# Kernel tuning notes

Measured on AMD Instinct MI355X. Metric: run time of the kernel, lower is better.

## Reference

```python
import jax, jax.numpy as jnp
import numpy as np

B, S, D, H, Dh, F = 1, 2048, 2048, 24, 128, 8192  # batch, seq, dim, heads, dim_head, ff hidden
SCALE = Dh ** -0.5


def _layernorm(x, g, b, eps=1e-5):
    mu = jnp.mean(x, axis=-1, keepdims=True)
    var = jnp.var(x, axis=-1, keepdims=True)
    return (x - mu) * jax.lax.rsqrt(var + eps) * g + b


def _rmsnorm(x, g, eps=1e-5):
    ms = jnp.mean(jnp.square(x), axis=-1, keepdims=True)
    return x * jax.lax.rsqrt(ms + eps) * g


def setup_inputs() -> dict:
    key = jax.random.key(0)
    ks = jax.random.split(key, 8)
    w = lambda k, sh: (jax.random.normal(k, sh, jnp.float32) * (1.0 / np.sqrt(sh[0]))).astype(jnp.float32)
    return {
        "x": jax.random.normal(ks[0], (B, S, D), jnp.float32),
        "ln_g": jnp.ones((D,), jnp.float32),
        "ln_b": jnp.zeros((D,), jnp.float32),
        "attn_g": jnp.ones((D,), jnp.float32),  # RingAttention prenorm (RMSNorm) gamma
        "Wq": w(ks[1], (D, H * Dh)),
        "Wk": w(ks[2], (D, H * Dh)),
        "Wv": w(ks[3], (D, H * Dh)),
        "Wo": w(ks[4], (H * Dh, D)),
        "W1": w(ks[5], (D, F)),
        "b1": jnp.zeros((F,), jnp.float32),
        "W2": w(ks[6], (F, D)),
        "b2": jnp.zeros((D,), jnp.float32),
    }


def reference(x, ln_g, ln_b, attn_g, Wq, Wk, Wv, Wo, W1, b1, W2, b2):
    # outer block LayerNorm
    x = _layernorm(x, ln_g, ln_b)

    # --- causal multi-head attention (math-equivalent to ring attention) ---
    h = _rmsnorm(x, attn_g)  # attention's internal prenorm
    q = (h @ Wq).reshape(B, S, H, Dh)
    k = (h @ Wk).reshape(B, S, H, Dh)
    v = (h @ Wv).reshape(B, S, H, Dh)
    scores = jnp.einsum("bqhd,bkhd->bhqk", q, k) * SCALE  # [B,H,S,S]
    causal = jnp.tril(jnp.ones((S, S), bool))
    scores = jnp.where(causal, scores, jnp.finfo(scores.dtype).min)
    attn = jax.nn.softmax(scores, axis=-1)
    o = jnp.einsum("bhqk,bkhd->bqhd", attn, v).reshape(B, S, H * Dh)
    x = o @ Wo + x  # residual

    # --- feedforward + residual ---
    x = jax.nn.gelu(x @ W1 + b1) @ W2 + b2 + x
    return x
```

## Files before the change

kernel.cpp:

```cpp
#include <hip/hip_runtime.h>
#include <hip/hip_bf16.h>

#define Sq 2048
#define Dm 2048
#define HDim 3072
#define QKVDim 9216
#define NH 24
#define DH 128
#define FF 8192
#define ATT_SCALE 0.08838834764831845f

using bf16 = __hip_bfloat16;
typedef __attribute__((ext_vector_type(8))) short bf16x8;
typedef __attribute__((ext_vector_type(4))) float f32x4;
typedef unsigned int u32;
typedef unsigned long long u64;
typedef __attribute__((ext_vector_type(4))) u32 u32x4;

__device__ __forceinline__ void gload_lds16(const void* g, void* l) {
    __builtin_amdgcn_global_load_lds(
        (const __attribute__((address_space(1))) void*)g,
        (__attribute__((address_space(3))) void*)l, 16, 0, 0);
}

__global__ __launch_bounds__(256) void ln_rms_kernel(
    const float* __restrict__ x, const float* __restrict__ g, const float* __restrict__ b,
    const float* __restrict__ ag, float* __restrict__ xnf, bf16* __restrict__ h)
{
    __shared__ float redA[4], redB[4], redC[4];
    int row = blockIdx.x;
    int t = threadIdx.x;
    int lane = t & 63, wid = t >> 6;
    const float* xr = x + (size_t)row * Dm;

    float v[8];
    float sum = 0.f, ssq = 0.f;
#pragma unroll
    for (int i = 0; i < 8; i++) {
        float f = xr[t + 256 * i];
        v[i] = f; sum += f; ssq += f * f;
    }
#pragma unroll
    for (int off = 32; off > 0; off >>= 1) {
        sum += __shfl_down(sum, off);
        ssq += __shfl_down(ssq, off);
    }
    if (lane == 0) { redA[wid] = sum; redB[wid] = ssq; }
    __syncthreads();
    sum = redA[0] + redA[1] + redA[2] + redA[3];
    ssq = redB[0] + redB[1] + redB[2] + redB[3];
    float mu = sum * (1.f / Dm);
    float var = ssq * (1.f / Dm) - mu * mu;
    float rstd = rsqrtf(var + 1e-5f);

    float xn[8];
    float s2 = 0.f;
#pragma unroll
    for (int i = 0; i < 8; i++) {
        int col = t + 256 * i;
        float xv = (v[i] - mu) * rstd * g[col] + b[col];
        xn[i] = xv;
        xnf[(size_t)row * Dm + col] = xv;
        s2 += xv * xv;
    }
#pragma unroll
    for (int off = 32; off > 0; off >>= 1) s2 += __shfl_down(s2, off);
    if (lane == 0) redC[wid] = s2;
    __syncthreads();
    s2 = redC[0] + redC[1] + redC[2] + redC[3];
    float rms = rsqrtf(s2 * (1.f / Dm) + 1e-5f);
#pragma unroll
    for (int i = 0; i < 8; i++) {
        int col = t + 256 * i;
        h[(size_t)row * Dm + col] = __float2bfloat16(xn[i] * rms * ag[col]);
    }
}

__global__ __launch_bounds__(256) void transpose_cvt_kernel(
    const float* __restrict__ W, bf16* __restrict__ Wt, int K, int N)
{
    __shared__ float tile[32][36];
    int n0 = blockIdx.x * 32, k0 = blockIdx.y * 32;
    int t = threadIdx.x;
    int r = t >> 3, c4 = (t & 7) * 4;
    f32x4 v = *reinterpret_cast<const f32x4*>(W + (size_t)(k0 + r) * N + n0 + c4);
    *reinterpret_cast<f32x4*>(&tile[r][c4]) = v;
    __syncthreads();
    int nr = t >> 3, kc = (t & 7) * 4;
    bf16 o4[4];
    o4[0] = __float2bfloat16(tile[kc + 0][nr]);
    o4[1] = __float2bfloat16(tile[kc + 1][nr]);
    o4[2] = __float2bfloat16(tile[kc + 2][nr]);
    o4[3] = __float2bfloat16(tile[kc + 3][nr]);
    *reinterpret_cast<u64*>(Wt + (size_t)(n0 + nr) * K + k0 + kc) = *reinterpret_cast<const u64*>(o4);
}

__global__ __launch_bounds__(256) void transpose_cvt3_kernel(
    const float* __restrict__ Wa, const float* __restrict__ Wb, const float* __restrict__ Wc,
    bf16* __restrict__ Wt, int K, int N)
{
    __shared__ float tile[32][36];
    const float* W = blockIdx.z == 0 ? Wa : (blockIdx.z == 1 ? Wb : Wc);
    bf16* dst = Wt + (size_t)blockIdx.z * N * K;
    int n0 = blockIdx.x * 32, k0 = blockIdx.y * 32;
    int t = threadIdx.x;
    int r = t >> 3, c4 = (t & 7) * 4;
    f32x4 v = *reinterpret_cast<const f32x4*>(W + (size_t)(k0 + r) * N + n0 + c4);
    *reinterpret_cast<f32x4*>(&tile[r][c4]) = v;
    __syncthreads();
    int nr = t >> 3, kc = (t & 7) * 4;
    bf16 o4[4];
    o4[0] = __float2bfloat16(tile[kc + 0][nr]);
    o4[1] = __float2bfloat16(tile[kc + 1][nr]);
    o4[2] = __float2bfloat16(tile[kc + 2][nr]);
    o4[3] = __float2bfloat16(tile[kc + 3][nr]);
    *reinterpret_cast<u64*>(dst + (size_t)(n0 + nr) * K + k0 + kc) = *reinterpret_cast<const u64*>(o4);
}

__global__ __launch_bounds__(256) void cvt_prefill_kernel(
    const float* __restrict__ xnf, const float* __restrict__ bias,
    bf16* __restrict__ hb, float* __restrict__ o, int N)
{
    int i = (blockIdx.x * 256 + threadIdx.x) * 8;
    int col = i % N;
    f32x4 a = *reinterpret_cast<const f32x4*>(xnf + i);
    f32x4 b = *reinterpret_cast<const f32x4*>(xnf + i + 4);
    bf16 r[8];
#pragma unroll
    for (int j = 0; j < 4; j++) { r[j] = __float2bfloat16(a[j]); r[4 + j] = __float2bfloat16(b[j]); }
    *reinterpret_cast<u32x4*>(hb + i) = *reinterpret_cast<const u32x4*>(r);
    f32x4 b0 = *reinterpret_cast<const f32x4*>(bias + col);
    f32x4 b1v = *reinterpret_cast<const f32x4*>(bias + col + 4);
    f32x4 o0 = {a[0] + b0[0], a[1] + b0[1], a[2] + b0[2], a[3] + b0[3]};
    f32x4 o1 = {b[0] + b1v[0], b[1] + b1v[1], b[2] + b1v[2], b[3] + b1v[3]};
    *reinterpret_cast<f32x4*>(o + i) = o0;
    *reinterpret_cast<f32x4*>(o + i + 4) = o1;
}

template <int EPI>
__global__ __launch_bounds__(256, 4) void gemm_kernel(
    const bf16* __restrict__ A, const bf16* __restrict__ Bt,
    int M, int N, int K, int Ksplit,
    bf16* Cb, float* Cf, const float* __restrict__ bias)
{
    __shared__ __align__(16) bf16 As[128 * 64];
    __shared__ __align__(16) bf16 Bs[128 * 64];
    int m0 = blockIdx.y * 128, n0 = blockIdx.x * 128;
    int kbeg = blockIdx.z * Ksplit, kend = kbeg + Ksplit;
    int tid = threadIdx.x;
    int lane = tid & 63, w = tid >> 6;
    int wr = w >> 1, wc = w & 1;
    int l15 = lane & 15, lhi = lane >> 4;

    int srow = lane >> 3;
    int scol = ((lane & 7) ^ (lane >> 3)) * 8;

    const f32x4 zero4 = {0.f, 0.f, 0.f, 0.f};
    f32x4 acc[4][4];
#pragma unroll
    for (int m = 0; m < 4; m++)
#pragma unroll
        for (int n = 0; n < 4; n++) acc[m][n] = zero4;

    for (int k0 = kbeg; k0 < kend; k0 += 64) {
        __syncthreads();
#pragma unroll
        for (int c = 0; c < 4; c++) {
            int row = w * 32 + c * 8 + srow;
            gload_lds16(A + (size_t)(m0 + row) * K + k0 + scol,
                        (char*)As + w * 4096 + c * 1024);
            gload_lds16(Bt + (size_t)(n0 + row) * K + k0 + scol,
                        (char*)Bs + w * 4096 + c * 1024);
        }
        __syncthreads();
#pragma unroll
        for (int ks = 0; ks < 2; ks++) {
            bf16x8 af[4], bfr[4];
#pragma unroll
            for (int m = 0; m < 4; m++) {
                int r = wr * 64 + m * 16 + l15;
                af[m] = *reinterpret_cast<const bf16x8*>(
                    &As[r * 64 + (((ks << 2) + lhi) ^ (r & 7)) * 8]);
            }
#pragma unroll
            for (int n = 0; n < 4; n++) {
                int r = wc * 64 + n * 16 + l15;
                bfr[n] = *reinterpret_cast<const bf16x8*>(
                    &Bs[r * 64 + (((ks << 2) + lhi) ^ (r & 7)) * 8]);
            }
#pragma unroll
            for (int m = 0; m < 4; m++)
#pragma unroll
                for (int n = 0; n < 4; n++)
                    acc[m][n] = __builtin_amdgcn_mfma_f32_16x16x32_bf16(af[m], bfr[n], acc[m][n], 0, 0, 0);
        }
    }

#pragma unroll
    for (int m = 0; m < 4; m++) {
        int row = m0 + wr * 64 + m * 16 + lhi * 4;
#pragma unroll
        for (int n = 0; n < 4; n++) {
            int col = n0 + wc * 64 + n * 16 + l15;
#pragma unroll
            for (int j = 0; j < 4; j++) {
                float vv = acc[m][n][j];
                size_t idx = (size_t)(row + j) * N + col;
                if (EPI == 0) {
                    Cb[idx] = __float2bfloat16(vv);
                } else if (EPI == 2) {
                    float o = vv + bias[col];
                    float u = 1.5957691216057308f * (o + 0.044715f * o * o * o);
                    Cb[idx] = __float2bfloat16(o / (1.0f + __expf(-u)));
                } else {
                    atomicAdd(&Cf[idx], vv);
                }
            }
        }
    }
}

__global__ __launch_bounds__(256) void attn_kernel(
    const bf16* __restrict__ qkv, bf16* __restrict__ o)
{
    __shared__ __align__(16) bf16 VtF[2][128 * 72];
    __shared__ __align__(16) bf16 Pl[4][16][72];
    int rank = blockIdx.x;
    int qb = (Sq / 64 - 1) - rank / NH;
    int head = rank % NH;
    const bf16* q = qkv + head * DH;
    const bf16* k = qkv + HDim + head * DH;
    const bf16* v = qkv + 2 * HDim + head * DH;
    int tid = threadIdx.x, lane = tid & 63, w = tid >> 6;
    int l15 = lane & 15, lhi = lane >> 4;
    int qrow0 = qb * 64 + w * 16;

    bf16x8 aq[4];
    const bf16* qbase = q + (size_t)(qrow0 + l15) * QKVDim;
#pragma unroll
    for (int kk = 0; kk < 4; kk++)
        aq[kk] = *reinterpret_cast<const bf16x8*>(qbase + kk * 32 + lhi * 8);

    const bf16* kbase = k + (size_t)l15 * QKVDim + lhi * 8;

    int vkv = lhi * 2 + (w & 1) + (w >> 1) * 8;
    int vd0 = l15 * 8;
    int vxr = l15 & 7;
    const bf16* vbase = v + (size_t)vkv * QKVDim + vd0;

    const f32x4 zero4 = {0.f, 0.f, 0.f, 0.f};
    f32x4 acc_o[8];
#pragma unroll
    for (int db = 0; db < 8; db++) acc_o[db] = zero4;
    float mrow[4], lrow[4];
#pragma unroll
    for (int r = 0; r < 4; r++) { mrow[r] = -1e30f; lrow[r] = 0.f; }

    int nt = qb + 1;
    bf16x8 bk[4][4], vreg[4];

#pragma unroll
    for (int nb = 0; nb < 4; nb++)
#pragma unroll
        for (int kk = 0; kk < 4; kk++)
            bk[nb][kk] = *reinterpret_cast<const bf16x8*>(
                kbase + (size_t)(nb * 16) * QKVDim + kk * 32);
#pragma unroll
    for (int i = 0; i < 4; i++)
        vreg[i] = *reinterpret_cast<const bf16x8*>(vbase + (size_t)(i * 16) * QKVDim);
#pragma unroll
    for (int i = 0; i < 4; i++) {
        int kv = vkv + i * 16, vb = kv >> 3, kr = kv & 7;
#pragma unroll
        for (int j = 0; j < 8; j++)
            VtF[0][(vd0 + j) * 72 + ((vb ^ vxr) << 3) + kr] = ((const bf16*)&vreg[i])[j];
    }
    __syncthreads();

    for (int kb = 0; kb < nt; kb++) {
        int kv0 = kb * 64, p = kb & 1;
        bool pref = (kb + 1 < nt);
        size_t nref = (size_t)(kv0 + 64) * QKVDim;
        if (pref) {
#pragma unroll
            for (int i = 0; i < 4; i++)
                vreg[i] = *reinterpret_cast<const bf16x8*>(
                    vbase + nref + (size_t)(i * 16) * QKVDim);
        }

        f32x4 sacc[4];
#pragma unroll
        for (int nb = 0; nb < 4; nb++) {
            sacc[nb] = zero4;
#pragma unroll
            for (int kk = 0; kk < 4; kk++)
                sacc[nb] = __builtin_amdgcn_mfma_f32_16x16x32_bf16(aq[kk], bk[nb][kk], sacc[nb], 0, 0, 0);
        }

        if (pref) {
#pragma unroll
            for (int nb = 0; nb < 4; nb++)
#pragma unroll
                for (int kk = 0; kk < 4; kk++)
                    bk[nb][kk] = *reinterpret_cast<const bf16x8*>(
                        kbase + nref + (size_t)(nb * 16) * QKVDim + kk * 32);
        }

        bool diag = (kb == qb);
        float sv[4][4];
        float pm[4];
#pragma unroll
        for (int r = 0; r < 4; r++) pm[r] = -1e30f;
#pragma unroll
        for (int nb = 0; nb < 4; nb++) {
            int kvc = kv0 + nb * 16 + l15;
#pragma unroll
            for (int r = 0; r < 4; r++) {
                int qr = qrow0 + lhi * 4 + r;
                float s = sacc[nb][r] * ATT_SCALE;
                if (diag && kvc > qr) s = -1e30f;
                sv[nb][r] = s;
                pm[r] = fmaxf(pm[r], s);
            }
        }
#pragma unroll
        for (int off = 1; off < 16; off <<= 1)
#pragma unroll
            for (int r = 0; r < 4; r++)
                pm[r] = fmaxf(pm[r], __shfl_xor(pm[r], off));

        float ls[4];
#pragma unroll
        for (int r = 0; r < 4; r++) {
            float mnew = fmaxf(mrow[r], pm[r]);
            float sc = __expf(mrow[r] - mnew);
            mrow[r] = mnew;
            lrow[r] *= sc;
#pragma unroll
            for (int db = 0; db < 8; db++) acc_o[db][r] *= sc;
            float lsr = 0.f;
#pragma unroll
            for (int nb = 0; nb < 4; nb++) {
                float pp = __expf(sv[nb][r] - mnew);
                sv[nb][r] = pp;
                lsr += pp;
            }
            ls[r] = lsr;
        }
#pragma unroll
        for (int off = 1; off < 16; off <<= 1)
#pragma unroll
            for (int r = 0; r < 4; r++)
                ls[r] += __shfl_xor(ls[r], off);
#pragma unroll
        for (int r = 0; r < 4; r++) lrow[r] += ls[r];

#pragma unroll
        for (int nb = 0; nb < 4; nb++)
#pragma unroll
            for (int r = 0; r < 4; r++)
                Pl[w][lhi * 4 + r][nb * 16 + l15] = __float2bfloat16(sv[nb][r]);

#pragma unroll
        for (int ks = 0; ks < 2; ks++) {
            bf16x8 ap = *reinterpret_cast<const bf16x8*>(&Pl[w][l15][ks * 32 + lhi * 8]);
#pragma unroll
            for (int db = 0; db < 8; db++) {
                int dv = db * 16 + l15;
                int blk = (ks * 4 + lhi) ^ ((dv >> 3) & 7);
                bf16x8 bv = *reinterpret_cast<const bf16x8*>(&VtF[p][dv * 72 + blk * 8]);
                acc_o[db] = __builtin_amdgcn_mfma_f32_16x16x32_bf16(ap, bv, acc_o[db], 0, 0, 0);
            }
        }

        __syncthreads();
        if (pref) {
#pragma unroll
            for (int i = 0; i < 4; i++) {
                int kv = vkv + i * 16, vb = kv >> 3, kr = kv & 7;
#pragma unroll
                for (int j = 0; j < 8; j++)
                    VtF[p ^ 1][(vd0 + j) * 72 + ((vb ^ vxr) << 3) + kr] = ((const bf16*)&vreg[i])[j];
            }
            __syncthreads();
        }
    }

#pragma unroll
    for (int db = 0; db < 8; db++)
#pragma unroll
        for (int r = 0; r < 4; r++) {
            int qr = qrow0 + lhi * 4 + r;
            float val = acc_o[db][r] / lrow[r];
            o[(size_t)qr * HDim + head * DH + db * 16 + l15] = __float2bfloat16(val);
        }
}

extern "C" void kernel_launch(void* const* d_in, const int* in_sizes, int n_in,
                              void* d_out, int out_size, void* d_ws, size_t ws_size,
                              hipStream_t stream)
{
    const float* x     = (const float*)d_in[0];
    const float* ln_g  = (const float*)d_in[1];
    const float* ln_b  = (const float*)d_in[2];
    const float* attng = (const float*)d_in[3];
    const float* Wq    = (const float*)d_in[4];
    const float* Wk    = (const float*)d_in[5];
    const float* Wv    = (const float*)d_in[6];
    const float* Wo    = (const float*)d_in[7];
    const float* W1    = (const float*)d_in[8];
    const float* b1    = (const float*)d_in[9];
    const float* W2    = (const float*)d_in[10];
    const float* b2    = (const float*)d_in[11];
    float* out = (float*)d_out;
    char* ws = (char*)d_ws;

    bf16*  wbuf = (bf16*)(ws + 0);
    float* xnf  = (float*)(ws + 39845888);
    bf16*  hbuf = (bf16*)(ws + 56623104);
    bf16*  qkv  = (bf16*)(ws + 65011712);
    bf16*  ob_  = (bf16*)(ws + 102760448);
    bf16*  gb_  = qkv;

    ln_rms_kernel<<<Sq, 256, 0, stream>>>(x, ln_g, ln_b, attng, xnf, hbuf);

    transpose_cvt3_kernel<<<dim3(HDim / 32, Dm / 32, 3), 256, 0, stream>>>(
        Wq, Wk, Wv, wbuf, Dm, HDim);
    gemm_kernel<0><<<dim3(QKVDim / 128, Sq / 128, 1), 256, 0, stream>>>(
        hbuf, wbuf, Sq, QKVDim, Dm, Dm, qkv, nullptr, nullptr);

    attn_kernel<<<dim3(NH * Sq / 64), 256, 0, stream>>>(qkv, ob_);

    transpose_cvt_kernel<<<dim3(Dm / 32, HDim / 32), 256, 0, stream>>>(Wo, wbuf, HDim, Dm);
    gemm_kernel<4><<<dim3(Dm / 128, Sq / 128, 2), 256, 0, stream>>>(
        ob_, wbuf, Sq, Dm, HDim, HDim / 2, nullptr, xnf, nullptr);
    cvt_prefill_kernel<<<(Sq * Dm) / (256 * 8), 256, 0, stream>>>(xnf, b2, hbuf, out, Dm);

    transpose_cvt_kernel<<<dim3(FF / 32, Dm / 32), 256, 0, stream>>>(W1, wbuf, Dm, FF);
    gemm_kernel<2><<<dim3(FF / 128, Sq / 128, 1), 256, 0, stream>>>(
        hbuf, wbuf, Sq, FF, Dm, Dm, gb_, nullptr, b1);

    transpose_cvt_kernel<<<dim3(Dm / 32, FF / 32), 256, 0, stream>>>(W2, wbuf, FF, Dm);
    gemm_kernel<4><<<dim3(Dm / 128, Sq / 128, 2), 256, 0, stream>>>(
        gb_, wbuf, Sq, Dm, FF, FF / 2, nullptr, out, nullptr);
}
```

Baseline: 493.3 us.

## Stage K tiles into swizzled LDS via async global-to-LDS loads in attention

The attention kernel used to hold the next K tile in 16 vector registers per lane, loaded straight from global memory. It now double-buffers K in a new XOR-swizzled LDS buffer, filled with global_load_lds DMA, and reads the MFMA operands from LDS. The Pl row pitch is padded from 72 to 76 to change bank mapping. This frees registers and should improve occupancy and coalescing. In exchange it uses more LDS and adds a waitcnt before each barrier. The V prefetch is issued twice, a redundant leftover that adds extra global loads.

```diff
diff --git a/kernel.cpp b/kernel.cpp
--- a/kernel.cpp
+++ b/kernel.cpp
@@ -223,8 +223,9 @@
 __global__ __launch_bounds__(256) void attn_kernel(
     const bf16* __restrict__ qkv, bf16* __restrict__ o)
 {
+    __shared__ __align__(16) bf16 KsF[2][64 * 128];
     __shared__ __align__(16) bf16 VtF[2][128 * 72];
-    __shared__ __align__(16) bf16 Pl[4][16][72];
+    __shared__ __align__(16) bf16 Pl[4][16][76];
     int rank = blockIdx.x;
     int qb = (Sq / 64 - 1) - rank / NH;
     int head = rank % NH;
@@ -241,8 +242,7 @@
     for (int kk = 0; kk < 4; kk++)
         aq[kk] = *reinterpret_cast<const bf16x8*>(qbase + kk * 32 + lhi * 8);
 
-    const bf16* kbase = k + (size_t)l15 * QKVDim + lhi * 8;
-
+    int krow_st = w * 16;
     int vkv = lhi * 2 + (w & 1) + (w >> 1) * 8;
     int vd0 = l15 * 8;
     int vxr = l15 & 7;
@@ -256,54 +256,67 @@
 #pragma unroll
     for (int r = 0; r < 4; r++) { mrow[r] = -1e30f; lrow[r] = 0.f; }
 
-    int nt = qb + 1;
-    bf16x8 bk[4][4], vreg[4];
-
-#pragma unroll
-    for (int nb = 0; nb < 4; nb++)
-#pragma unroll
-        for (int kk = 0; kk < 4; kk++)
-            bk[nb][kk] = *reinterpret_cast<const bf16x8*>(
-                kbase + (size_t)(nb * 16) * QKVDim + kk * 32);
-#pragma unroll
-    for (int i = 0; i < 4; i++)
-        vreg[i] = *reinterpret_cast<const bf16x8*>(vbase + (size_t)(i * 16) * QKVDim);
-#pragma unroll
-    for (int i = 0; i < 4; i++) {
-        int kv = vkv + i * 16, vb = kv >> 3, kr = kv & 7;
-#pragma unroll
-        for (int j = 0; j < 8; j++)
-            VtF[0][(vd0 + j) * 72 + ((vb ^ vxr) << 3) + kr] = ((const bf16*)&vreg[i])[j];
-    }
-    __syncthreads();
-
-    for (int kb = 0; kb < nt; kb++) {
-        int kv0 = kb * 64, p = kb & 1;
-        bool pref = (kb + 1 < nt);
-        size_t nref = (size_t)(kv0 + 64) * QKVDim;
+    {
+#pragma unroll
+        for (int c = 0; c < 4; c++) {
+            int row = krow_st + c * 4 + lhi;
+            int cb = l15 ^ (row & 7);
+            gload_lds16(k + (size_t)row * QKVDim + cb * 8,
+                        (char*)&KsF[0][0] + w * 4096 + c * 1024);
+        }
+#pragma unroll
+        for (int i = 0; i < 4; i++) {
+            int kv = vkv + i * 16;
+            bf16x8 vv = *reinterpret_cast<const bf16x8*>(vbase + (size_t)(i * 16) * QKVDim);
+            int vb = kv >> 3, kr = kv & 7;
+#pragma unroll
+            for (int j = 0; j < 8; j++)
+                VtF[0][(vd0 + j) * 72 + ((vb ^ vxr) << 3) + kr] = ((const bf16*)&vv)[j];
+        }
+        asm volatile("s_waitcnt vmcnt(0)" ::: "memory");
+        __syncthreads();
+    }
+
+    for (int kb = 0; kb <= qb; kb++) {
+        int kv0 = kb * 64;
+        int p = kb & 1;
+        bf16x8 vreg[4];
+        bool pref = (kb < qb);
         if (pref) {
+            int nv0 = kv0 + 64;
+#pragma unroll
+            for (int c = 0; c < 4; c++) {
+                int row = krow_st + c * 4 + lhi;
+                int cb = l15 ^ (row & 7);
+                gload_lds16(k + (size_t)(nv0 + row) * QKVDim + cb * 8,
+                            (char*)&KsF[p ^ 1][0] + w * 4096 + c * 1024);
+            }
 #pragma unroll
             for (int i = 0; i < 4; i++)
                 vreg[i] = *reinterpret_cast<const bf16x8*>(
-                    vbase + nref + (size_t)(i * 16) * QKVDim);
+                    vbase + (size_t)(nv0 + i * 16) * QKVDim - (size_t)vkv * QKVDim
+                    + (size_t)vkv * QKVDim);
+        }
+        if (pref) {
+            int nv0 = kv0 + 64;
+#pragma unroll
+            for (int i = 0; i < 4; i++)
+                vreg[i] = *reinterpret_cast<const bf16x8*>(
+                    v + (size_t)(nv0 + vkv + i * 16) * QKVDim + vd0);
         }
 
         f32x4 sacc[4];
 #pragma unroll
         for (int nb = 0; nb < 4; nb++) {
             sacc[nb] = zero4;
-#pragma unroll
-            for (int kk = 0; kk < 4; kk++)
-                sacc[nb] = __builtin_amdgcn_mfma_f32_16x16x32_bf16(aq[kk], bk[nb][kk], sacc[nb], 0, 0, 0);
-        }
-
-        if (pref) {
-#pragma unroll
-            for (int nb = 0; nb < 4; nb++)
-#pragma unroll
-                for (int kk = 0; kk < 4; kk++)
-                    bk[nb][kk] = *reinterpret_cast<const bf16x8*>(
-                        kbase + nref + (size_t)(nb * 16) * QKVDim + kk * 32);
+            int krow = nb * 16 + l15;
+#pragma unroll
+            for (int kk = 0; kk < 4; kk++) {
+                const char* kp = (const char*)&KsF[p][0] + krow * 256 +
+                                 ((kk * 64 + lhi * 16) ^ ((krow & 7) << 4));
+                bf16x8 bk = *reinterpret_cast<const bf16x8*>(kp);
+                sacc[nb] = __builtin_amdgcn_mfma_f32_16x16x32_bf16(aq[kk], bk, sacc[nb], 0, 0, 0);
+            }
         }
 
         bool diag = (kb == qb);
@@ -377,11 +390,13 @@
         if (pref) {
 #pragma unroll
             for (int i = 0; i < 4; i++) {
-                int kv = vkv + i * 16, vb = kv >> 3, kr = kv & 7;
+                int kv = vkv + i * 16;
+                int vb = kv >> 3, kr = kv & 7;
 #pragma unroll
                 for (int j = 0; j < 8; j++)
                     VtF[p ^ 1][(vd0 + j) * 72 + ((vb ^ vxr) << 3) + kr] = ((const bf16*)&vreg[i])[j];
             }
+            asm volatile("s_waitcnt vmcnt(0)" ::: "memory");
             __syncthreads();
         }
     }
```

Result: faster. 464.3 us (-5.9%).
